# Performance work log

Hardware: AMD Instinct MI355X
Metric: run time of the kernel (lower is better)

## Reference

```python
import jax, jax.numpy as jnp
import numpy as np

NUM_CLASSES = 32
N = 2_000_000
EPS = jnp.float32(np.finfo(np.float32).eps)  # torch.finfo(torch.float32).eps


def setup_inputs() -> dict:
    key = jax.random.key(0)
    k1, k2 = jax.random.split(key)
    y_true = jax.random.normal(k1, (N, NUM_CLASSES), dtype=jnp.float32)
    y_pred = jax.random.normal(k2, (N, NUM_CLASSES), dtype=jnp.float32)
    confusion_matrix = jnp.zeros((NUM_CLASSES, NUM_CLASSES), dtype=jnp.float32)
    return {"y_true": y_true, "y_pred": y_pred, "confusion_matrix": confusion_matrix}


def reference(y_true, y_pred, confusion_matrix):
    C = confusion_matrix.shape[0]
    # update(): argmax then scatter-accumulate into the confusion matrix
    t = jnp.argmax(y_true, axis=1)  # [N] int
    p = jnp.argmax(y_pred, axis=1)  # [N] int
    flat = t * C + p                # flattened (row, col) index
    hist = jnp.zeros((C * C,), dtype=jnp.float32).at[flat].add(1.0)
    cm = confusion_matrix + hist.reshape(C, C)
    # compute() with average='macro'
    tp = jnp.diag(cm)
    predicted_positives = jnp.sum(cm, axis=0)
    precision_per_class = tp / (predicted_positives + EPS)
    return jnp.mean(precision_per_class)
```

## Files before the change

kernel.cpp:

```cpp
#include <hip/hip_runtime.h>

#define C 32
#define BINS (C * C)
#define TILE_ROWS 256
#define ROWPAD 36
#define NBLOCKS 1024
#define FLT_EPS 1.1920928955078125e-07f

typedef float v4f __attribute__((ext_vector_type(4)));

__global__ __launch_bounds__(256) void hist_kernel(
    const float* __restrict__ yt,
    const float* __restrict__ yp,
    unsigned int* __restrict__ partial,
    int N)
{
    __shared__ float buf[TILE_ROWS * ROWPAD];
    __shared__ unsigned int lhist[BINS];
    const int t = threadIdx.x;
    for (int i = t; i < BINS; i += 256) lhist[i] = 0u;

    const int numTiles = (N + TILE_ROWS - 1) / TILE_ROWS;
    int ti_reg = 0;

    for (int tile = blockIdx.x; tile < numTiles; tile += gridDim.x) {
        const size_t row0 = (size_t)tile * TILE_ROWS;
        const int rowsValid = min(TILE_ROWS, N - (int)row0);

        {
            const v4f* src = (const v4f*)(yt + row0 * C);
            #pragma unroll
            for (int q = 0; q < 8; ++q) {
                const int lin = q * 256 + t;
                const int r = lin >> 3, m = lin & 7;
                if (r < rowsValid) {
                    v4f v = __builtin_nontemporal_load(src + lin);
                    *(v4f*)&buf[r * ROWPAD + m * 4] = v;
                }
            }
        }
        __syncthreads();
        if (t < rowsValid) {
            float bv = -__builtin_inff(); int bi = C;
            const float* rowp = &buf[t * ROWPAD];
            #pragma unroll
            for (int j = 0; j < C; ++j) {
                const int c = (j + t) & (C - 1);
                const float v = rowp[c];
                const bool better = (v > bv) || (v == bv && c < bi);
                bv = better ? v : bv;
                bi = better ? c : bi;
            }
            ti_reg = bi;
        }
        __syncthreads();

        {
            const v4f* src = (const v4f*)(yp + row0 * C);
            #pragma unroll
            for (int q = 0; q < 8; ++q) {
                const int lin = q * 256 + t;
                const int r = lin >> 3, m = lin & 7;
                if (r < rowsValid) {
                    v4f v = __builtin_nontemporal_load(src + lin);
                    *(v4f*)&buf[r * ROWPAD + m * 4] = v;
                }
            }
        }
        __syncthreads();
        if (t < rowsValid) {
            float bv = -__builtin_inff(); int bi = C;
            const float* rowp = &buf[t * ROWPAD];
            #pragma unroll
            for (int j = 0; j < C; ++j) {
                const int c = (j + t) & (C - 1);
                const float v = rowp[c];
                const bool better = (v > bv) || (v == bv && c < bi);
                bv = better ? v : bv;
                bi = better ? c : bi;
            }
            atomicAdd(&lhist[ti_reg * C + bi], 1u);
        }
        __syncthreads();
    }

    if (t < C) {
        unsigned int cs = 0;
        #pragma unroll
        for (int i = 0; i < C; ++i) cs += lhist[i * C + t];
        partial[(size_t)blockIdx.x * 64 + t] = cs;
        partial[(size_t)blockIdx.x * 64 + C + t] = lhist[t * C + t];
    }
}

__global__ __launch_bounds__(1024) void finalize_kernel(
    const unsigned int* __restrict__ partial,
    const float* __restrict__ cm_in,
    float* __restrict__ out)
{
    __shared__ float sums[16][64];
    const int tid = threadIdx.x;
    const int col = tid & 63;
    const int kg = tid >> 6;

    unsigned int s = 0;
    #pragma unroll 8
    for (int k = kg * (NBLOCKS / 16); k < (kg + 1) * (NBLOCKS / 16); ++k)
        s += partial[(size_t)k * 64 + col];
    sums[kg][col] = (float)s;
    __syncthreads();

    if (tid < 64) {
        float tot = 0.0f;
        #pragma unroll
        for (int g = 0; g < 16; ++g) tot += sums[g][tid];
        sums[0][tid] = tot;
    }
    __syncthreads();

    if (tid < C) {
        const int j = tid;
        float pp = sums[0][j];
        float tp = sums[0][C + j];
        float cmcol = 0.0f;
        #pragma unroll
        for (int i = 0; i < C; ++i) cmcol += cm_in[i * C + j];
        pp += cmcol;
        tp += cm_in[j * C + j];
        float prec = tp / (pp + FLT_EPS);
        #pragma unroll
        for (int m = 1; m < C; m <<= 1) prec += __shfl_xor(prec, m);
        if (j == 0) out[0] = prec * (1.0f / (float)C);
    }
}

extern "C" void kernel_launch(void* const* d_in, const int* in_sizes, int n_in,
                              void* d_out, int out_size, void* d_ws, size_t ws_size,
                              hipStream_t stream)
{
    const float* yt = (const float*)d_in[0];
    const float* yp = (const float*)d_in[1];
    const float* cm = (const float*)d_in[2];
    float* out = (float*)d_out;
    const int N = in_sizes[0] / C;

    unsigned int* partial = (unsigned int*)d_ws;

    hist_kernel<<<NBLOCKS, 256, 0, stream>>>(yt, yp, partial, N);
    finalize_kernel<<<1, 1024, 0, stream>>>(partial, cm, out);
}
```

Measured before the change: 480.5 us.

## Replace LDS-staged argmax with register-prefetched 8-lane shuffle argmax

```diff
diff --git a/kernel.cpp b/kernel.cpp
--- a/kernel.cpp
+++ b/kernel.cpp
@@ -2,94 +2,82 @@
 
 #define C 32
 #define BINS (C * C)
-#define TILE_ROWS 256
-#define ROWPAD 36
-#define NBLOCKS 1024
+#define NBLOCKS 2048
+#define NTHREADS 256
+#define ROWS_PER_STEP ((NBLOCKS * NTHREADS) / 8)
 #define FLT_EPS 1.1920928955078125e-07f
 
 typedef float v4f __attribute__((ext_vector_type(4)));
 
-__global__ __launch_bounds__(256) void hist_kernel(
+__device__ __forceinline__ unsigned long long pack_best4(v4f v, int base) {
+    unsigned long long best = 0ull;
+    #pragma unroll
+    for (int k = 0; k < 4; ++k) {
+        unsigned int u = __float_as_uint(v[k]);
+        unsigned int key = u ^ ((unsigned int)((int)u >> 31) | 0x80000000u);
+        unsigned long long p =
+            ((unsigned long long)key << 32) | (unsigned int)(63 - (base + k));
+        best = (p > best) ? p : best;
+    }
+    return best;
+}
+
+__global__ __launch_bounds__(NTHREADS) void hist_kernel(
     const float* __restrict__ yt,
     const float* __restrict__ yp,
     unsigned int* __restrict__ partial,
     int N)
 {
-    __shared__ float buf[TILE_ROWS * ROWPAD];
     __shared__ unsigned int lhist[BINS];
     const int t = threadIdx.x;
-    for (int i = t; i < BINS; i += 256) lhist[i] = 0u;
+    for (int i = t; i < BINS; i += NTHREADS) lhist[i] = 0u;
+    __syncthreads();
 
-    const int numTiles = (N + TILE_ROWS - 1) / TILE_ROWS;
-    int ti_reg = 0;
-
-    for (int tile = blockIdx.x; tile < numTiles; tile += gridDim.x) {
-        const size_t row0 = (size_t)tile * TILE_ROWS;
-        const int rowsValid = min(TILE_ROWS, N - (int)row0);
-
-        {
-            const v4f* src = (const v4f*)(yt + row0 * C);
-            #pragma unroll
-            for (int q = 0; q < 8; ++q) {
-                const int lin = q * 256 + t;
-                const int r = lin >> 3, m = lin & 7;
-                if (r < rowsValid) {
-                    v4f v = __builtin_nontemporal_load(src + lin);
-                    *(v4f*)&buf[r * ROWPAD + m * 4] = v;
-                }
-            }
-        }
-        __syncthreads();
-        if (t < rowsValid) {
-            float bv = -__builtin_inff(); int bi = C;
-            const float* rowp = &buf[t * ROWPAD];
-            #pragma unroll
-            for (int j = 0; j < C; ++j) {
-                const int c = (j + t) & (C - 1);
-                const float v = rowp[c];
-                const bool better = (v > bv) || (v == bv && c < bi);
-                bv = better ? v : bv;
-                bi = better ? c : bi;
-            }
-            ti_reg = bi;
-        }
-        __syncthreads();
-
-        {
-            const v4f* src = (const v4f*)(yp + row0 * C);
-            #pragma unroll
-            for (int q = 0; q < 8; ++q) {
-                const int lin = q * 256 + t;
-                const int r = lin >> 3, m = lin & 7;
-                if (r < rowsValid) {
-                    v4f v = __builtin_nontemporal_load(src + lin);
-                    *(v4f*)&buf[r * ROWPAD + m * 4] = v;
-                }
-            }
-        }
-        __syncthreads();
-        if (t < rowsValid) {
-            float bv = -__builtin_inff(); int bi = C;
-            const float* rowp = &buf[t * ROWPAD];
-            #pragma unroll
-            for (int j = 0; j < C; ++j) {
-                const int c = (j + t) & (C - 1);
-                const float v = rowp[c];
-                const bool better = (v > bv) || (v == bv && c < bi);
-                bv = better ? v : bv;
-                bi = better ? c : bi;
-            }
-            atomicAdd(&lhist[ti_reg * C + bi], 1u);
-        }
-        __syncthreads();
+    const int lane8 = t & 7;
+    long long row = (long long)((blockIdx.x * NTHREADS + t) >> 3);
+    bool valid = row < N;
+    v4f a, b;
+    if (valid) {
+        a = __builtin_nontemporal_load(((const v4f*)(yt + row * C)) + lane8);
+        b = __builtin_nontemporal_load(((const v4f*)(yp + row * C)) + lane8);
     }
 
-    if (t < C) {
+    while (valid) {
+        const long long nrow = row + ROWS_PER_STEP;
+        const bool nvalid = nrow < N;
+        v4f na, nb;
+        if (nvalid) {
+            na = __builtin_nontemporal_load(((const v4f*)(yt + nrow * C)) + lane8);
+            nb = __builtin_nontemporal_load(((const v4f*)(yp + nrow * C)) + lane8);
+        }
+
+        unsigned long long bt = pack_best4(a, lane8 * 4);
+        unsigned long long bp = pack_best4(b, lane8 * 4);
+        #pragma unroll
+        for (int m = 1; m < 8; m <<= 1) {
+            unsigned long long ot = __shfl_xor(bt, m);
+            bt = (ot > bt) ? ot : bt;
+            unsigned long long op = __shfl_xor(bp, m);
+            bp = (op > bp) ? op : bp;
+        }
+        if (lane8 == 0) {
+            const int ti = 63 - (int)(bt & 63ull);
+            const int pi = 63 - (int)(bp & 63ull);
+            atomicAdd(&lhist[ti * C + pi], 1u);
+        }
+
+        row = nrow; valid = nvalid; a = na; b = nb;
+    }
+
+    __syncthreads();
+    if (t < 32) {
         unsigned int cs = 0;
         #pragma unroll
         for (int i = 0; i < C; ++i) cs += lhist[i * C + t];
         partial[(size_t)blockIdx.x * 64 + t] = cs;
-        partial[(size_t)blockIdx.x * 64 + C + t] = lhist[t * C + t];
+    } else if (t < 64) {
+        const int j = t - 32;
+        partial[(size_t)blockIdx.x * 64 + t] = lhist[j * C + j];
     }
 }
 
@@ -146,6 +134,6 @@
 
     unsigned int* partial = (unsigned int*)d_ws;
 
-    hist_kernel<<<NBLOCKS, 256, 0, stream>>>(yt, yp, partial, N);
+    hist_kernel<<<NBLOCKS, NTHREADS, 0, stream>>>(yt, yp, partial, N);
     finalize_kernel<<<1, 1024, 0, stream>>>(partial, cm, out);
 }
```

Result: faster. 461.3 us (-4.0%).
